# Optimization experiments

Measured on AMD Instinct MI355X. Metric: run time of the kernel, lower is better.

## Reference

```python
import jax, jax.numpy as jnp
import numpy as np

B, T, C, H = 4, 1024, 1024, 16
D = C // H
EPS = 1e-5


def _ln(x, g, b):
    mu = jnp.mean(x, axis=-1, keepdims=True)
    var = jnp.mean((x - mu) ** 2, axis=-1, keepdims=True)
    return (x - mu) * jax.lax.rsqrt(var + EPS) * g + b


def _attn(xq, xkv, wq, wk, wv, wo, bo, mask):
    # wq/wk/wv/wo: [C, C] (in, out). Dropout is identity in eval mode.
    Bq, Tq, _ = xq.shape
    Tk = xkv.shape[1]
    q = (xq @ wq).reshape(Bq, Tq, H, D)
    k = (xkv @ wk).reshape(Bq, Tk, H, D)
    v = (xkv @ wv).reshape(Bq, Tk, H, D)
    scores = jnp.einsum('bqhd,bkhd->bhqk', q, k) / jnp.sqrt(jnp.float32(D))
    if mask is not None:
        scores = jnp.where(mask == 0, -jnp.inf, scores)
    p = jax.nn.softmax(scores, axis=-1)
    out = jnp.einsum('bhqk,bkhd->bqhd', p, v).reshape(Bq, Tq, C)
    return out @ wo + bo


def setup_inputs() -> dict:
    key = jax.random.key(0)
    ks = jax.random.split(key, 20)
    s = 0.02
    inp = {
        'x': jax.random.normal(ks[0], (B, T, C), jnp.float32),
        'encoder_out': jax.random.normal(ks[1], (B, T, C), jnp.float32),
        'sa_wq': jax.random.normal(ks[2], (C, C), jnp.float32) * s,
        'sa_wk': jax.random.normal(ks[3], (C, C), jnp.float32) * s,
        'sa_wv': jax.random.normal(ks[4], (C, C), jnp.float32) * s,
        'sa_wo': jax.random.normal(ks[5], (C, C), jnp.float32) * s,
        'sa_bo': jnp.zeros((C,), jnp.float32),
        'ca_wq': jax.random.normal(ks[6], (C, C), jnp.float32) * s,
        'ca_wk': jax.random.normal(ks[7], (C, C), jnp.float32) * s,
        'ca_wv': jax.random.normal(ks[8], (C, C), jnp.float32) * s,
        'ca_wo': jax.random.normal(ks[9], (C, C), jnp.float32) * s,
        'ca_bo': jnp.zeros((C,), jnp.float32),
        'ff_w1': jax.random.normal(ks[10], (C, 4 * C), jnp.float32) * s,
        'ff_b1': jnp.zeros((4 * C,), jnp.float32),
        'ff_w2': jax.random.normal(ks[11], (4 * C, C), jnp.float32) * s,
        'ff_b2': jnp.zeros((C,), jnp.float32),
        'ln1_g': jnp.ones((C,), jnp.float32), 'ln1_b': jnp.zeros((C,), jnp.float32),
        'ln2_g': jnp.ones((C,), jnp.float32), 'ln2_b': jnp.zeros((C,), jnp.float32),
        'ln3_g': jnp.ones((C,), jnp.float32), 'ln3_b': jnp.zeros((C,), jnp.float32),
        'tgt_mask': jnp.tril(jnp.ones((T, T), jnp.int32))[None, None],  # [1,1,T,T] causal
        'src_mask': jnp.ones((B, 1, 1, T), jnp.int32),
    }
    return inp


def reference(x, encoder_out, sa_wq, sa_wk, sa_wv, sa_wo, sa_bo,
              ca_wq, ca_wk, ca_wv, ca_wo, ca_bo,
              ff_w1, ff_b1, ff_w2, ff_b2,
              ln1_g, ln1_b, ln2_g, ln2_b, ln3_g, ln3_b,
              tgt_mask, src_mask):
    # self-attention (masked) + residual
    x = x + _attn(_ln(x, ln1_g, ln1_b), _ln(x, ln1_g, ln1_b),
                  sa_wq, sa_wk, sa_wv, sa_wo, sa_bo, tgt_mask)
    # cross-attention + residual (only src_mask applied to scores)
    h = _ln(x, ln2_g, ln2_b)
    x = x + _attn(h, encoder_out, ca_wq, ca_wk, ca_wv, ca_wo, ca_bo, src_mask)
    # FFN + residual
    h = _ln(x, ln3_g, ln3_b)
    x = x + (jax.nn.relu(h @ ff_w1 + ff_b1) @ ff_w2 + ff_b2)
    return x
```

## Files before the change

kernel.cpp:

```cpp
#include <hip/hip_runtime.h>

typedef __bf16 bf16_t;
typedef __bf16 bf16x4 __attribute__((ext_vector_type(4)));
typedef __bf16 bf16x8 __attribute__((ext_vector_type(8)));
typedef float  f32x4  __attribute__((ext_vector_type(4)));

#define LN_EPS 1e-5f

__device__ __forceinline__ void g2l16(const bf16_t* g, bf16_t* l) {
    __builtin_amdgcn_global_load_lds(
        (const __attribute__((address_space(1))) void*)g,
        (__attribute__((address_space(3))) void*)l, 16, 0, 0);
}

__global__ __launch_bounds__(256) void cvt_kernel(
    const float* __restrict__ x, bf16_t* __restrict__ y)
{
    int i = blockIdx.x * 256 + threadIdx.x;
    f32x4 v = ((const f32x4*)x)[i];
    bf16x4 o = { (bf16_t)v.x, (bf16_t)v.y, (bf16_t)v.z, (bf16_t)v.w };
    ((bf16x4*)y)[i] = o;
}

__global__ __launch_bounds__(256) void zero_kernel(float* __restrict__ p)
{
    f32x4 z = { 0.f, 0.f, 0.f, 0.f };
    ((f32x4*)p)[blockIdx.x * 256 + threadIdx.x] = z;
}

struct WT16 {
    const float* src[16]; bf16_t* dst[16];
    int srcN[16]; int dstK[16]; int k0b[16]; int n0b[16];
};

__global__ __launch_bounds__(256) void wt16_kernel(WT16 p)
{
    const int z = blockIdx.z;
    const float* W = p.src[z];
    bf16_t* Wt = p.dst[z];
    const int N = p.srcN[z], Kd = p.dstK[z];
    const int n0 = p.n0b[z] + blockIdx.x * 64, k0 = p.k0b[z] + blockIdx.y * 64;
    __shared__ float ts[64][65];
    const int tid = threadIdx.x;
#pragma unroll
    for (int it = 0; it < 4; ++it) {
        int f = tid + it * 256;
        int row = f >> 4, c4 = (f & 15) * 4;
        f32x4 v = *(const f32x4*)(W + (size_t)(k0 + row) * N + n0 + c4);
        ts[row][c4 + 0] = v.x; ts[row][c4 + 1] = v.y;
        ts[row][c4 + 2] = v.z; ts[row][c4 + 3] = v.w;
    }
    __syncthreads();
#pragma unroll
    for (int it = 0; it < 4; ++it) {
        int f = tid + it * 256;
        int nrow = f >> 4, k4 = (f & 15) * 4;
        bf16x4 o = { (bf16_t)ts[k4 + 0][nrow], (bf16_t)ts[k4 + 1][nrow],
                     (bf16_t)ts[k4 + 2][nrow], (bf16_t)ts[k4 + 3][nrow] };
        *(bf16x4*)(Wt + (size_t)(n0 + nrow) * Kd + k0 + k4) = o;
    }
}

__global__ __launch_bounds__(256) void ln_kernel(
    const float* __restrict__ x, const float* __restrict__ g,
    const float* __restrict__ b, bf16_t* __restrict__ y)
{
    const int row = blockIdx.x;
    const int tid = threadIdx.x;
    const f32x4* xr = (const f32x4*)(x + (size_t)row * 1024);
    f32x4 v = xr[tid];
    float s  = v.x + v.y + v.z + v.w;
    float s2 = v.x*v.x + v.y*v.y + v.z*v.z + v.w*v.w;
#pragma unroll
    for (int off = 1; off < 64; off <<= 1) {
        s  += __shfl_xor(s,  off, 64);
        s2 += __shfl_xor(s2, off, 64);
    }
    __shared__ float ws_[4], ws2_[4];
    const int wave = tid >> 6, lane = tid & 63;
    if (lane == 0) { ws_[wave] = s; ws2_[wave] = s2; }
    __syncthreads();
    s  = ws_[0] + ws_[1] + ws_[2] + ws_[3];
    s2 = ws2_[0] + ws2_[1] + ws2_[2] + ws2_[3];
    const float mu   = s  * (1.0f/1024.0f);
    const float var  = s2 * (1.0f/1024.0f) - mu*mu;
    const float rstd = rsqrtf(var + LN_EPS);
    f32x4 gv = ((const f32x4*)g)[tid];
    f32x4 bv = ((const f32x4*)b)[tid];
    f32x4 o  = (v - mu) * rstd * gv + bv;
    bf16x4 ob = { (bf16_t)o.x, (bf16_t)o.y, (bf16_t)o.z, (bf16_t)o.w };
    ((bf16x4*)(y + (size_t)row * 1024))[tid] = ob;
}

template<int BN, int DEPTH, int OUT_BF16, int HAS_BIAS, int DO_RELU, int HAS_RES,
         int SPLITK>
__global__ __launch_bounds__(256) void gemm_bf16(
    const bf16_t* __restrict__ A, const bf16_t* __restrict__ Bt,
    const float* __restrict__ bias, const float* __restrict__ res,
    void* __restrict__ out, int M, int N, int K)
{
    constexpr int NT = BN / 32;
    __shared__ __align__(16) bf16_t As[2][DEPTH][128 * 32];
    __shared__ __align__(16) bf16_t Bs[2][DEPTH][BN * 32];

    const int tid  = threadIdx.x;
    const int wave = tid >> 6, lane = tid & 63;
    const int q    = lane >> 4, r = lane & 15;
    const int wm   = wave >> 1, wn = wave & 1;

    const int nbx  = gridDim.x;
    const int id   = blockIdx.y * nbx + blockIdx.x;
    const int mper = gridDim.y >> 3;
    const int jj   = id >> 3;
    const int bm   = (id & 7) * mper + jj / nbx;
    const int bn   = jj % nbx;
    const int m0   = bm * 128, n0 = bn * BN;

    const int srow = lane >> 2;
    const int schk = ((lane & 3) ^ ((lane >> 3) & 3)) * 8;
    const int rsw  = ((r >> 1) & 3) * 8;

    auto stage = [&](int buf, int kk) {
#pragma unroll
        for (int s = 0; s < DEPTH; ++s) {
#pragma unroll
            for (int t = 0; t < 2; ++t) {
                int rowA = wave * 32 + t * 16;
                g2l16(A + (size_t)(m0 + rowA + srow) * K + kk + s * 32 + schk,
                      &As[buf][s][rowA * 32]);
            }
#pragma unroll
            for (int t = 0; t < BN / 64; ++t) {
                int rowB = wave * (BN / 4) + t * 16;
                g2l16(Bt + (size_t)(n0 + rowB + srow) * K + kk + s * 32 + schk,
                      &Bs[buf][s][rowB * 32]);
            }
        }
    };

    f32x4 acc[4][NT] = {};
    constexpr int STEP = 32 * DEPTH;
    const int Kc    = K / SPLITK;
    const int kbase = (SPLITK > 1) ? blockIdx.z * Kc : 0;
    stage(0, kbase);

    for (int kk = 0; kk < Kc; kk += STEP) {
        const int cur = (kk / STEP) & 1;
        __syncthreads();
        if (kk + STEP < Kc) stage(cur ^ 1, kbase + kk + STEP);
#pragma unroll
        for (int s = 0; s < DEPTH; ++s) {
            bf16x8 af[4], bfr[NT];
#pragma unroll
            for (int i = 0; i < 4; ++i)
                af[i] = *(const bf16x8*)&As[cur][s][(wm * 64 + i * 16 + r) * 32 + (q * 8 ^ rsw)];
#pragma unroll
            for (int j = 0; j < NT; ++j)
                bfr[j] = *(const bf16x8*)&Bs[cur][s][(wn * 16 * NT + j * 16 + r) * 32 + (q * 8 ^ rsw)];
#pragma unroll
            for (int i = 0; i < 4; ++i)
#pragma unroll
                for (int j = 0; j < NT; ++j)
                    acc[i][j] = __builtin_amdgcn_mfma_f32_16x16x32_bf16(af[i], bfr[j], acc[i][j], 0, 0, 0);
        }
    }

#pragma unroll
    for (int i = 0; i < 4; ++i)
#pragma unroll
        for (int j = 0; j < NT; ++j)
#pragma unroll
            for (int e = 0; e < 4; ++e) {
                int row = m0 + wm * 64 + i * 16 + q * 4 + e;
                int col = n0 + wn * 16 * NT + j * 16 + r;
                float v = acc[i][j][e];
                if (SPLITK == 1) {
                    if (HAS_BIAS) v += bias[col];
                    if (DO_RELU)  v = v > 0.0f ? v : 0.0f;
                    if (HAS_RES)  v += res[(size_t)row * N + col];
                    if (OUT_BF16) ((bf16_t*)out)[(size_t)row * N + col] = (bf16_t)v;
                    else          ((float*)out)[(size_t)row * N + col] = v;
                } else {
                    if (blockIdx.z == 0) {
                        if (HAS_BIAS) v += bias[col];
                        if (HAS_RES)  v += res[(size_t)row * N + col];
                    }
                    atomicAdd(&((float*)out)[(size_t)row * N + col], v);
                }
            }
}

__global__ __launch_bounds__(256) void gemm_qkv3(
    const bf16_t* __restrict__ Aq, const bf16_t* __restrict__ Akv,
    const bf16_t* __restrict__ Wt3,
    bf16_t* __restrict__ outq, bf16_t* __restrict__ outk,
    bf16_t* __restrict__ vt)
{
    const int K = 1024;
    __shared__ __align__(16) bf16_t As[2][128 * 32];
    __shared__ __align__(16) bf16_t Bs[2][128 * 32];

    const int tid  = threadIdx.x;
    const int wave = tid >> 6, lane = tid & 63;
    const int q    = lane >> 4, r = lane & 15;
    const int wm   = wave >> 1, wn = wave & 1;

    const int nbx  = gridDim.x;
    const int id   = blockIdx.y * nbx + blockIdx.x;
    const int mper = gridDim.y >> 3;
    const int jj   = id >> 3;
    const int bm   = (id & 7) * mper + jj / nbx;
    const int bn   = jj % nbx;
    const int m0   = bm * 128, n0 = bn * 128;
    const int grp  = bn >> 3;
    const bf16_t* A = (grp == 0) ? Aq : Akv;

    const int srow = lane >> 2;
    const int schk = ((lane & 3) ^ ((lane >> 3) & 3)) * 8;
    const int rsw  = ((r >> 1) & 3) * 8;

    auto stage = [&](int buf, int kk) {
#pragma unroll
        for (int t = 0; t < 2; ++t) {
            int row = wave * 32 + t * 16;
            g2l16(A   + (size_t)(m0 + row + srow) * K + kk + schk, &As[buf][row * 32]);
            g2l16(Wt3 + (size_t)(n0 + row + srow) * K + kk + schk, &Bs[buf][row * 32]);
        }
    };

    f32x4 acc[4][4] = {};
    stage(0, 0);

    for (int kk = 0; kk < K; kk += 32) {
        const int cur = (kk >> 5) & 1;
        __syncthreads();
        if (kk + 32 < K) stage(cur ^ 1, kk + 32);

        bf16x8 af[4], bfr[4];
#pragma unroll
        for (int i = 0; i < 4; ++i)
            af[i] = *(const bf16x8*)&As[cur][(wm * 64 + i * 16 + r) * 32 + (q * 8 ^ rsw)];
#pragma unroll
        for (int j = 0; j < 4; ++j)
            bfr[j] = *(const bf16x8*)&Bs[cur][(wn * 64 + j * 16 + r) * 32 + (q * 8 ^ rsw)];
#pragma unroll
        for (int i = 0; i < 4; ++i)
#pragma unroll
            for (int j = 0; j < 4; ++j)
                acc[i][j] = __builtin_amdgcn_mfma_f32_16x16x32_bf16(af[i], bfr[j], acc[i][j], 0, 0, 0);
    }

    if (grp < 2) {
        bf16_t* o = (grp == 0) ? outq : outk;
        const float sc = (grp == 0) ? 0.125f : 1.0f;
        const int c0 = n0 - grp * 1024;
#pragma unroll
        for (int i = 0; i < 4; ++i)
#pragma unroll
            for (int j = 0; j < 4; ++j)
#pragma unroll
                for (int e = 0; e < 4; ++e) {
                    int row = m0 + wm * 64 + i * 16 + q * 4 + e;
                    int col = c0 + wn * 64 + j * 16 + r;
                    o[(size_t)row * 1024 + col] = (bf16_t)(acc[i][j][e] * sc);
                }
    } else {
#pragma unroll
        for (int i = 0; i < 4; ++i)
#pragma unroll
            for (int j = 0; j < 4; ++j) {
                int c = (n0 - 2048) + wn * 64 + j * 16 + r;
                int hh = c >> 6, d = c & 63;
                int row0 = m0 + wm * 64 + i * 16 + q * 4;
                int bb = row0 >> 10, t = row0 & 1023;
                bf16x4 pk = { (bf16_t)acc[i][j][0], (bf16_t)acc[i][j][1],
                              (bf16_t)acc[i][j][2], (bf16_t)acc[i][j][3] };
                *(bf16x4*)&vt[((size_t)((bb << 4) + hh) * 64 + d) * 1024 + t] = pk;
            }
    }
}

template<int CAUSAL>
__global__ __launch_bounds__(256) void attn_mfma_kernel(
    const bf16_t* __restrict__ Qp, const bf16_t* __restrict__ Kp,
    const bf16_t* __restrict__ VTp, bf16_t* __restrict__ Op)
{
    const int T = 1024;
    const int LP = 72;
    __shared__ __align__(16) bf16_t Ps[128 * LP];
    __shared__ __align__(16) bf16_t Ks[2][2][64 * 32];
    __shared__ __align__(16) bf16_t Vs[2][2][64 * 32];

    const int id  = blockIdx.x + 8 * (blockIdx.y + 16 * blockIdx.z);
    const int jj  = id >> 3;
    const int pr  = (id & 7) * 8 + (jj >> 3);
    const int qt  = jj & 7;
    const int h   = pr & 15, b = pr >> 4;

    const int tid  = threadIdx.x;
    const int wave = tid >> 6, lane = tid & 63;
    const int q    = lane >> 4, r = lane & 15;
    const int srow = lane >> 2, schk = (lane & 3) * 8;

    const bf16_t* Kb = Kp + (size_t)(b * T) * 1024 + h * 64;
    const bf16_t* Vb = VTp + (size_t)((b * 16 + h) * 64) * 1024;

    auto stageKV = [&](int buf, int kt) {
#pragma unroll
        for (int ks = 0; ks < 2; ++ks) {
            g2l16(Kb + (size_t)(kt * 64 + wave * 16 + srow) * 1024 + ks * 32 + schk,
                  &Ks[buf][ks][wave * 16 * 32]);
            g2l16(Vb + (size_t)(wave * 16 + srow) * 1024 + kt * 64 + ks * 32 + schk,
                  &Vs[buf][ks][wave * 16 * 32]);
        }
    };

    {
        const bf16_t* Qb = Qp + (size_t)(b * T + qt * 128) * 1024 + h * 64;
#pragma unroll
        for (int it = 0; it < 4; ++it) {
            int f = tid + it * 256;
            int row = f >> 3, c8 = (f & 7) * 8;
            *(bf16x8*)&Ps[row * LP + c8] = *(const bf16x8*)(Qb + (size_t)row * 1024 + c8);
        }
    }
    __syncthreads();
    bf16x8 qa[2][2];
#pragma unroll
    for (int mt = 0; mt < 2; ++mt)
#pragma unroll
        for (int ks = 0; ks < 2; ++ks)
            qa[mt][ks] = *(const bf16x8*)&Ps[(wave * 32 + mt * 16 + r) * LP + ks * 32 + q * 8];

    const bf16_t one_b = (bf16_t)1.0f;
    const bf16x8 ones = { one_b, one_b, one_b, one_b, one_b, one_b, one_b, one_b };

    f32x4 o[2][4] = {};
    f32x4 ol[2] = {};

    const int nk = CAUSAL ? (2 * qt + 2) : 16;
    stageKV(0, 0);

    for (int kt = 0; kt < nk; ++kt) {
        const int cur = kt & 1;
        __syncthreads();
        if (kt + 1 < nk) stageKV(cur ^ 1, kt + 1);

        f32x4 s[2][4] = {};
#pragma unroll
        for (int ks = 0; ks < 2; ++ks)
#pragma unroll
            for (int nt = 0; nt < 4; ++nt) {
                bf16x8 kb = *(const bf16x8*)&Ks[cur][ks][(nt * 16 + r) * 32 + q * 8];
#pragma unroll
                for (int mt = 0; mt < 2; ++mt)
                    s[mt][nt] = __builtin_amdgcn_mfma_f32_16x16x32_bf16(qa[mt][ks], kb, s[mt][nt], 0, 0, 0);
            }

        if (CAUSAL) {
#pragma unroll
            for (int mt = 0; mt < 2; ++mt) {
                const int r0 = qt * 128 + wave * 32 + mt * 16;
                if (kt * 64 + 63 > r0) {
#pragma unroll
                    for (int nt = 0; nt < 4; ++nt) {
                        int kg = kt * 64 + nt * 16 + r;
#pragma unroll
                        for (int i2 = 0; i2 < 4; ++i2)
                            if (kg > r0 + q * 4 + i2) s[mt][nt][i2] = -INFINITY;
                    }
                }
            }
        }

#pragma unroll
        for (int mt = 0; mt < 2; ++mt)
#pragma unroll
            for (int nt = 0; nt < 4; ++nt)
#pragma unroll
                for (int i2 = 0; i2 < 4; ++i2)
                    Ps[(wave * 32 + mt * 16 + q * 4 + i2) * LP + nt * 16 + r] =
                        (bf16_t)__expf(s[mt][nt][i2]);

#pragma unroll
        for (int ks = 0; ks < 2; ++ks) {
            bf16x8 pa[2];
#pragma unroll
            for (int mt = 0; mt < 2; ++mt)
                pa[mt] = *(const bf16x8*)&Ps[(wave * 32 + mt * 16 + r) * LP + ks * 32 + q * 8];
#pragma unroll
            for (int dt = 0; dt < 4; ++dt) {
                bf16x8 vb = *(const bf16x8*)&Vs[cur][ks][(dt * 16 + r) * 32 + q * 8];
#pragma unroll
                for (int mt = 0; mt < 2; ++mt)
                    o[mt][dt] = __builtin_amdgcn_mfma_f32_16x16x32_bf16(pa[mt], vb, o[mt][dt], 0, 0, 0);
            }
#pragma unroll
            for (int mt = 0; mt < 2; ++mt)
                ol[mt] = __builtin_amdgcn_mfma_f32_16x16x32_bf16(pa[mt], ones, ol[mt], 0, 0, 0);
        }
    }

    bf16_t* Ob = Op + (size_t)(b * T + qt * 128 + wave * 32) * 1024 + h * 64;
#pragma unroll
    for (int mt = 0; mt < 2; ++mt) {
        f32x4 inv;
#pragma unroll
        for (int i2 = 0; i2 < 4; ++i2) inv[i2] = 1.0f / ol[mt][i2];
#pragma unroll
        for (int dt = 0; dt < 4; ++dt)
#pragma unroll
            for (int i2 = 0; i2 < 4; ++i2)
                Ob[(size_t)(mt * 16 + q * 4 + i2) * 1024 + dt * 16 + r] = (bf16_t)(o[mt][dt][i2] * inv[i2]);
    }
}

extern "C" void kernel_launch(void* const* d_in, const int* in_sizes, int n_in,
                              void* d_out, int out_size, void* d_ws, size_t ws_size,
                              hipStream_t stream)
{
    const float* x     = (const float*)d_in[0];
    const float* enc   = (const float*)d_in[1];
    const float* sa_wq = (const float*)d_in[2];
    const float* sa_wk = (const float*)d_in[3];
    const float* sa_wv = (const float*)d_in[4];
    const float* sa_wo = (const float*)d_in[5];
    const float* sa_bo = (const float*)d_in[6];
    const float* ca_wq = (const float*)d_in[7];
    const float* ca_wk = (const float*)d_in[8];
    const float* ca_wv = (const float*)d_in[9];
    const float* ca_wo = (const float*)d_in[10];
    const float* ca_bo = (const float*)d_in[11];
    const float* ff_w1 = (const float*)d_in[12];
    const float* ff_b1 = (const float*)d_in[13];
    const float* ff_w2 = (const float*)d_in[14];
    const float* ff_b2 = (const float*)d_in[15];
    const float* ln1_g = (const float*)d_in[16];
    const float* ln1_b = (const float*)d_in[17];
    const float* ln2_g = (const float*)d_in[18];
    const float* ln2_b = (const float*)d_in[19];
    const float* ln3_g = (const float*)d_in[20];
    const float* ln3_b = (const float*)d_in[21];

    float* out = (float*)d_out;
    char* ws = (char*)d_ws;
    const size_t MB = 1024 * 1024;
    bf16_t* w_s3  = (bf16_t*)(ws +  0 * MB);
    bf16_t* w_so  = (bf16_t*)(ws +  6 * MB);
    bf16_t* w_c3  = (bf16_t*)(ws +  8 * MB);
    bf16_t* w_co  = (bf16_t*)(ws + 14 * MB);
    bf16_t* w_f1  = (bf16_t*)(ws + 16 * MB);
    bf16_t* w_f2  = (bf16_t*)(ws + 24 * MB);
    bf16_t* b_enc = (bf16_t*)(ws + 32 * MB);
    bf16_t* b_ln  = (bf16_t*)(ws + 40 * MB);
    bf16_t* b_q   = (bf16_t*)(ws + 48 * MB);
    bf16_t* b_k   = (bf16_t*)(ws + 56 * MB);
    bf16_t* b_vt  = (bf16_t*)(ws + 64 * MB);
    bf16_t* b_at  = (bf16_t*)(ws + 72 * MB);
    float*  b_x1  = (float*) (ws + 80 * MB);
    float*  b_x2  = (float*) (ws + 48 * MB);
    bf16_t* b_h1  = (bf16_t*)(ws + 64 * MB);

    const int M = 4096;
    dim3 blk(256);

    zero_kernel<<<4096, blk, 0, stream>>>(out);

    WT16 wp;
    const float* srcs[8] = { sa_wq, sa_wk, sa_wv, sa_wo, ca_wq, ca_wk, ca_wv, ca_wo };
    bf16_t* dsts[8] = { w_s3, w_s3 + 1024*1024, w_s3 + 2048*1024, w_so,
                        w_c3, w_c3 + 1024*1024, w_c3 + 2048*1024, w_co };
    for (int z = 0; z < 8; ++z) {
        wp.src[z] = srcs[z]; wp.dst[z] = dsts[z];
        wp.srcN[z] = 1024; wp.dstK[z] = 1024; wp.k0b[z] = 0; wp.n0b[z] = 0;
    }
    for (int z = 8; z < 12; ++z) {
        wp.src[z] = ff_w1; wp.dst[z] = w_f1;
        wp.srcN[z] = 4096; wp.dstK[z] = 1024; wp.k0b[z] = 0; wp.n0b[z] = (z - 8) * 1024;
    }
    for (int z = 12; z < 16; ++z) {
        wp.src[z] = ff_w2; wp.dst[z] = w_f2;
        wp.srcN[z] = 1024; wp.dstK[z] = 4096; wp.k0b[z] = (z - 12) * 1024; wp.n0b[z] = 0;
    }
    wt16_kernel<<<dim3(16, 16, 16), blk, 0, stream>>>(wp);
    cvt_kernel<<<4096, blk, 0, stream>>>(enc, b_enc);

    ln_kernel<<<4096, blk, 0, stream>>>(x, ln1_g, ln1_b, b_ln);
    gemm_qkv3<<<dim3(24, 32), blk, 0, stream>>>(b_ln, b_ln, w_s3, b_q, b_k, b_vt);
    attn_mfma_kernel<1><<<dim3(8, 16, 4), blk, 0, stream>>>(b_q, b_k, b_vt, b_at);
    gemm_bf16<64,2,0,1,0,1,1><<<dim3(16, 32), blk, 0, stream>>>(
        b_at, w_so, sa_bo, x, b_x1, M, 1024, 1024);
    ln_kernel<<<4096, blk, 0, stream>>>(b_x1, ln2_g, ln2_b, b_ln);
    gemm_qkv3<<<dim3(24, 32), blk, 0, stream>>>(b_ln, b_enc, w_c3, b_q, b_k, b_vt);
    attn_mfma_kernel<0><<<dim3(8, 16, 4), blk, 0, stream>>>(b_q, b_k, b_vt, b_at);
    gemm_bf16<64,2,0,1,0,1,1><<<dim3(16, 32), blk, 0, stream>>>(
        b_at, w_co, ca_bo, b_x1, b_x2, M, 1024, 1024);
    ln_kernel<<<4096, blk, 0, stream>>>(b_x2, ln3_g, ln3_b, b_ln);
    gemm_bf16<128,1,1,1,1,0,1><<<dim3(32, 32), blk, 0, stream>>>(
        b_ln, w_f1, ff_b1, nullptr, b_h1, M, 4096, 1024);
    gemm_bf16<128,1,0,1,0,1,4><<<dim3(8, 32, 4), blk, 0, stream>>>(
        b_h1, w_f2, ff_b2, b_x2, out, M, 1024, 4096);
}
```

Baseline: 513.9 us.

## Replace atomic split-K FFN2 with two partial buffers and swizzle attention LDS

```diff
diff --git a/kernel.cpp b/kernel.cpp
--- a/kernel.cpp
+++ b/kernel.cpp
@@ -22,10 +22,14 @@
     ((bf16x4*)y)[i] = o;
 }
 
-__global__ __launch_bounds__(256) void zero_kernel(float* __restrict__ p)
-{
-    f32x4 z = { 0.f, 0.f, 0.f, 0.f };
-    ((f32x4*)p)[blockIdx.x * 256 + threadIdx.x] = z;
+__global__ __launch_bounds__(256) void add2_kernel(
+    const float* __restrict__ p0, const float* __restrict__ p1,
+    float* __restrict__ out)
+{
+    int i = blockIdx.x * 256 + threadIdx.x;
+    f32x4 a = ((const f32x4*)p0)[i];
+    f32x4 b = ((const f32x4*)p1)[i];
+    ((f32x4*)out)[i] = a + b;
 }
 
 struct WT16 {
@@ -97,7 +101,8 @@
 __global__ __launch_bounds__(256) void gemm_bf16(
     const bf16_t* __restrict__ A, const bf16_t* __restrict__ Bt,
     const float* __restrict__ bias, const float* __restrict__ res,
-    void* __restrict__ out, int M, int N, int K)
+    void* __restrict__ out, void* __restrict__ out2,
+    int M, int N, int K)
 {
     constexpr int NT = BN / 32;
     __shared__ __align__(16) bf16_t As[2][DEPTH][128 * 32];
@@ -165,6 +170,7 @@
         }
     }
 
+    float* po = (float*)((SPLITK > 1 && blockIdx.z != 0) ? out2 : out);
 #pragma unroll
     for (int i = 0; i < 4; ++i)
 #pragma unroll
@@ -185,7 +191,7 @@
                         if (HAS_BIAS) v += bias[col];
                         if (HAS_RES)  v += res[(size_t)row * N + col];
                     }
-                    atomicAdd(&((float*)out)[(size_t)row * N + col], v);
+                    po[(size_t)row * N + col] = v;
                 }
             }
 }
@@ -300,7 +306,9 @@
     const int tid  = threadIdx.x;
     const int wave = tid >> 6, lane = tid & 63;
     const int q    = lane >> 4, r = lane & 15;
-    const int srow = lane >> 2, schk = (lane & 3) * 8;
+    const int srow = lane >> 2;
+    const int schk = ((lane & 3) ^ ((lane >> 3) & 3)) * 8;
+    const int rsw  = ((r >> 1) & 3) * 8;
 
     const bf16_t* Kb = Kp + (size_t)(b * T) * 1024 + h * 64;
     const bf16_t* Vb = VTp + (size_t)((b * 16 + h) * 64) * 1024;
@@ -351,7 +359,7 @@
         for (int ks = 0; ks < 2; ++ks)
 #pragma unroll
             for (int nt = 0; nt < 4; ++nt) {
-                bf16x8 kb = *(const bf16x8*)&Ks[cur][ks][(nt * 16 + r) * 32 + q * 8];
+                bf16x8 kb = *(const bf16x8*)&Ks[cur][ks][(nt * 16 + r) * 32 + (q * 8 ^ rsw)];
 #pragma unroll
                 for (int mt = 0; mt < 2; ++mt)
                     s[mt][nt] = __builtin_amdgcn_mfma_f32_16x16x32_bf16(qa[mt][ks], kb, s[mt][nt], 0, 0, 0);
@@ -390,7 +398,7 @@
                 pa[mt] = *(const bf16x8*)&Ps[(wave * 32 + mt * 16 + r) * LP + ks * 32 + q * 8];
 #pragma unroll
             for (int dt = 0; dt < 4; ++dt) {
-                bf16x8 vb = *(const bf16x8*)&Vs[cur][ks][(dt * 16 + r) * 32 + q * 8];
+                bf16x8 vb = *(const bf16x8*)&Vs[cur][ks][(dt * 16 + r) * 32 + (q * 8 ^ rsw)];
 #pragma unroll
                 for (int mt = 0; mt < 2; ++mt)
                     o[mt][dt] = __builtin_amdgcn_mfma_f32_16x16x32_bf16(pa[mt], vb, o[mt][dt], 0, 0, 0);
@@ -460,11 +468,11 @@
     float*  b_x1  = (float*) (ws + 80 * MB);
     float*  b_x2  = (float*) (ws + 48 * MB);
     bf16_t* b_h1  = (bf16_t*)(ws + 64 * MB);
+    float*  p_sk0 = (float*) (ws +  0 * MB);
+    float*  p_sk1 = (float*) (ws + 32 * MB);
 
     const int M = 4096;
     dim3 blk(256);
-
-    zero_kernel<<<4096, blk, 0, stream>>>(out);
 
     WT16 wp;
     const float* srcs[8] = { sa_wq, sa_wk, sa_wv, sa_wo, ca_wq, ca_wk, ca_wv, ca_wo };
@@ -489,15 +497,16 @@
     gemm_qkv3<<<dim3(24, 32), blk, 0, stream>>>(b_ln, b_ln, w_s3, b_q, b_k, b_vt);
     attn_mfma_kernel<1><<<dim3(8, 16, 4), blk, 0, stream>>>(b_q, b_k, b_vt, b_at);
     gemm_bf16<64,2,0,1,0,1,1><<<dim3(16, 32), blk, 0, stream>>>(
-        b_at, w_so, sa_bo, x, b_x1, M, 1024, 1024);
+        b_at, w_so, sa_bo, x, b_x1, nullptr, M, 1024, 1024);
     ln_kernel<<<4096, blk, 0, stream>>>(b_x1, ln2_g, ln2_b, b_ln);
     gemm_qkv3<<<dim3(24, 32), blk, 0, stream>>>(b_ln, b_enc, w_c3, b_q, b_k, b_vt);
     attn_mfma_kernel<0><<<dim3(8, 16, 4), blk, 0, stream>>>(b_q, b_k, b_vt, b_at);
     gemm_bf16<64,2,0,1,0,1,1><<<dim3(16, 32), blk, 0, stream>>>(
-        b_at, w_co, ca_bo, b_x1, b_x2, M, 1024, 1024);
+        b_at, w_co, ca_bo, b_x1, b_x2, nullptr, M, 1024, 1024);
     ln_kernel<<<4096, blk, 0, stream>>>(b_x2, ln3_g, ln3_b, b_ln);
     gemm_bf16<128,1,1,1,1,0,1><<<dim3(32, 32), blk, 0, stream>>>(
-        b_ln, w_f1, ff_b1, nullptr, b_h1, M, 4096, 1024);
-    gemm_bf16<128,1,0,1,0,1,4><<<dim3(8, 32, 4), blk, 0, stream>>>(
-        b_h1, w_f2, ff_b2, b_x2, out, M, 1024, 4096);
-}
+        b_ln, w_f1, ff_b1, nullptr, b_h1, nullptr, M, 4096, 1024);
+    gemm_bf16<64,1,0,1,0,1,2><<<dim3(16, 32, 2), blk, 0, stream>>>(
+        b_h1, w_f2, ff_b2, b_x2, p_sk0, p_sk1, M, 1024, 4096);
+    add2_kernel<<<4096, blk, 0, stream>>>(p_sk0, p_sk1, out);
+}
```

Measured after the change: 486.1 us. 1.06x faster.
